# Kernel optimization log

Hardware: AMD Instinct MI355X
Metric: run time of the kernel (lower is better)

## Reference

```python
import jax, jax.numpy as jnp
import numpy as np

TT_SHAPES = [16, 16, 16, 16, 16, 16]
TT_RANKS = [1, 64, 64, 64, 64, 64, 1]
OUT_FEATURES = 4096  # 16*16*16
IN_FEATURES = 4096   # 16*16*16
N_TOKENS = 8192


def setup_inputs() -> dict:
    key = jax.random.key(0)
    ks = jax.random.split(key, len(TT_SHAPES) + 2)
    inp = {}
    for i in range(len(TT_SHAPES)):
        shape = (TT_RANKS[i], TT_SHAPES[i], TT_RANKS[i + 1])
        # xavier-uniform-like init
        fan = TT_RANKS[i] * TT_SHAPES[i] + TT_SHAPES[i] * TT_RANKS[i + 1]
        bound = float(np.sqrt(6.0 / fan))
        inp[f"core{i}"] = jax.random.uniform(ks[i], shape, jnp.float32, -bound, bound)
    inp["x"] = jax.random.normal(ks[-2], (N_TOKENS, IN_FEATURES), dtype=jnp.float32)
    b_bound = 1.0 / np.sqrt(IN_FEATURES)
    inp["b"] = jax.random.uniform(ks[-1], (OUT_FEATURES,), jnp.float32, -b_bound, b_bound)
    return inp


def _recover_weight(cores):
    # chain of reshape+matmul contractions, exactly as TTLinearR._recover_weight
    w = cores[0]
    for i in range(1, len(cores)):
        w = w.reshape(-1, TT_RANKS[i]) @ cores[i].reshape(TT_RANKS[i], -1)
    return w.reshape(OUT_FEATURES, IN_FEATURES)


def reference(x, core0, core1, core2, core3, core4, core5, b):
    w = _recover_weight([core0, core1, core2, core3, core4, core5])
    # F.linear(x, w, b) == x @ w.T + b
    return x @ w.T + b
```

## Files before the change

### kernel.cpp

```cpp
#include <hip/hip_runtime.h>


#define TOK 8192
#define DIN 4096
#define DOUT 4096
#define RNK 64

typedef __bf16 bf16x8 __attribute__((ext_vector_type(8)));
typedef float f32x4 __attribute__((ext_vector_type(4)));
typedef float f32x16 __attribute__((ext_vector_type(16)));

__device__ __forceinline__ unsigned short f2bf(float f) {
  unsigned int u = __float_as_uint(f);
  u += 0x7FFFu + ((u >> 16) & 1u);
  return (unsigned short)(u >> 16);
}

__global__ void chain1(const float* __restrict__ c0, const float* __restrict__ c1,
                       const float* __restrict__ c4, const float* __restrict__ c5,
                       float* __restrict__ S1, float* __restrict__ S3) {
  int b = blockIdx.x;
  if (b < 64) {
    int idx = b * 256 + threadIdx.x;
    int m = idx >> 10, n = idx & 1023;
    const float* a = c0 + m * 64;
    float acc = 0.f;
#pragma unroll
    for (int k = 0; k < 64; ++k) acc += a[k] * c1[k * 1024 + n];
    S1[idx] = acc;
  } else {
    int idx = (b - 64) * 256 + threadIdx.x;
    int m = idx >> 4, n = idx & 15;
    const float* a = c4 + m * 64;
    float acc = 0.f;
#pragma unroll
    for (int k = 0; k < 64; ++k) acc += a[k] * c5[k * 16 + n];
    S3[idx] = acc;
  }
}

__global__ void chain2(const float* __restrict__ S1, const float* __restrict__ c2,
                       const float* __restrict__ c3, const float* __restrict__ S3,
                       unsigned short* __restrict__ Abf, unsigned short* __restrict__ Bbf) {
  int b = blockIdx.x;
  if (b < 1024) {
    int idx = b * 256 + threadIdx.x;
    int m = idx >> 10, n = idx & 1023;
    const float* a = S1 + m * 64;
    float acc = 0.f;
#pragma unroll
    for (int k = 0; k < 64; ++k) acc += a[k] * c2[k * 1024 + n];
    Abf[idx] = f2bf(acc);
  } else {
    int idx = (b - 1024) * 256 + threadIdx.x;
    int m = idx >> 8, n = idx & 255;
    const float* a = c3 + m * 64;
    float acc = 0.f;
#pragma unroll
    for (int k = 0; k < 64; ++k) acc += a[k] * S3[k * 256 + n];
    Bbf[idx] = f2bf(acc);
  }
}

__global__ __launch_bounds__(512, 4)
void gemm1_s(const float* __restrict__ x, const unsigned short* __restrict__ Bbf,
             unsigned short* __restrict__ tb) {
  __shared__ float red[8 * 1024];

  const int tid = threadIdx.x;
  const int m0 = blockIdx.x * 16;
  const int lane = tid & 63, wv = tid >> 6;
  const int r = lane & 15, q = lane >> 4;
  const size_t xrow = (size_t)(m0 + r) * DIN;
  const int k0w = wv * 512;

  f32x4 acc[4];
#pragma unroll
  for (int j = 0; j < 4; ++j) acc[j] = (f32x4){0.f, 0.f, 0.f, 0.f};

#pragma unroll
  for (int st = 0; st < 16; ++st) {
    const int k0 = k0w + st * 32 + q * 8;
    float4 xa = *(const float4*)&x[xrow + k0];
    float4 xb = *(const float4*)&x[xrow + k0 + 4];
    bf16x8 a;
    a[0] = (__bf16)xa.x; a[1] = (__bf16)xa.y; a[2] = (__bf16)xa.z; a[3] = (__bf16)xa.w;
    a[4] = (__bf16)xb.x; a[5] = (__bf16)xb.y; a[6] = (__bf16)xb.z; a[7] = (__bf16)xb.w;
#pragma unroll
    for (int j = 0; j < 4; ++j) {
      bf16x8 b = *(const bf16x8*)&Bbf[(size_t)(j * 16 + r) * DIN + k0];
      acc[j] = __builtin_amdgcn_mfma_f32_16x16x32_bf16(a, b, acc[j], 0, 0, 0);
    }
  }

  float* myred = red + wv * 1024;
#pragma unroll
  for (int j = 0; j < 4; ++j)
#pragma unroll
    for (int g = 0; g < 4; ++g)
      myred[(q * 4 + g) * 64 + j * 16 + r] = acc[j][g];
  __syncthreads();

  const int o = tid * 2;
  float s0 = 0.f, s1 = 0.f;
#pragma unroll
  for (int w = 0; w < 8; ++w) {
    s0 += red[w * 1024 + o];
    s1 += red[w * 1024 + o + 1];
  }
  ushort2 h = {f2bf(s0), f2bf(s1)};
  *(ushort2*)&tb[(size_t)m0 * RNK + o] = h;
}

__global__ __launch_bounds__(256, 4)
void gemm2_s(const unsigned short* __restrict__ tb, const unsigned short* __restrict__ Abf,
             const float* __restrict__ bias, float* __restrict__ out) {
  const int tid = threadIdx.x;
  const int lane = tid & 63, wv = tid >> 6;
  const int l31 = lane & 31, hi = lane >> 5;
  const int n0 = blockIdx.x * 128;
  const int mb = blockIdx.y * 256;

  float bb[4];
#pragma unroll
  for (int n = 0; n < 4; ++n) bb[n] = bias[n0 + n * 32 + l31];

#pragma unroll 1
  for (int s = 0; s < 2; ++s) {
    const int m0 = mb + s * 128 + wv * 32;
    bf16x8 ta[4];
#pragma unroll
    for (int ks = 0; ks < 4; ++ks)
      ta[ks] = *(const bf16x8*)&tb[(size_t)(m0 + l31) * RNK + ks * 16 + hi * 8];

#pragma unroll 1
    for (int np = 0; np < 2; ++np) {
      f32x16 acc[2];
#pragma unroll
      for (int j = 0; j < 2; ++j)
#pragma unroll
        for (int e = 0; e < 16; ++e) acc[j][e] = 0.f;

#pragma unroll
      for (int ks = 0; ks < 4; ++ks) {
#pragma unroll
        for (int j = 0; j < 2; ++j) {
          const int nrow = n0 + (np * 2 + j) * 32 + l31;
          bf16x8 b = *(const bf16x8*)&Abf[(size_t)nrow * RNK + ks * 16 + hi * 8];
          acc[j] = __builtin_amdgcn_mfma_f32_32x32x16_bf16(ta[ks], b, acc[j], 0, 0, 0);
        }
      }

#pragma unroll
      for (int j = 0; j < 2; ++j) {
        const int col = n0 + (np * 2 + j) * 32 + l31;
        const float bj = bb[np * 2 + j];
#pragma unroll
        for (int reg = 0; reg < 16; ++reg) {
          const int rowt = (reg & 3) + 8 * (reg >> 2) + 4 * hi;
          out[(size_t)(m0 + rowt) * DOUT + col] = acc[j][reg] + bj;
        }
      }
    }
  }
}

extern "C" void kernel_launch(void* const* d_in, const int* in_sizes, int n_in,
                              void* d_out, int out_size, void* d_ws, size_t ws_size,
                              hipStream_t stream) {
  const float* c0 = (const float*)d_in[0];
  const float* c1 = (const float*)d_in[1];
  const float* c2 = (const float*)d_in[2];
  const float* c3 = (const float*)d_in[3];
  const float* c4 = (const float*)d_in[4];
  const float* c5 = (const float*)d_in[5];
  const float* x  = (const float*)d_in[6];
  const float* bias = (const float*)d_in[7];
  float* out = (float*)d_out;

  char* ws = (char*)d_ws;
  float*          S1  = (float*)(ws);
  float*          S3  = (float*)(ws + (1u << 16));
  unsigned short* Abf = (unsigned short*)(ws + (2u << 16));
  unsigned short* Bbf = (unsigned short*)(ws + (2u << 16) + (1u << 19));
  unsigned short* tbf = (unsigned short*)(ws + (2u << 16) + (2u << 19));

  chain1<<<128, 256, 0, stream>>>(c0, c1, c4, c5, S1, S3);
  chain2<<<2048, 256, 0, stream>>>(S1, c2, c3, S3, Abf, Bbf);
  gemm1_s<<<TOK / 16, 512, 0, stream>>>(x, Bbf, tbf);
  gemm2_s<<<dim3(DOUT / 128, TOK / 256), 256, 0, stream>>>(tbf, Abf, bias, out);
}
```

Measured before the change: 283.5 us.

## Software-pipeline gemm1 loads and stage gemm2 operands through padded LDS tiles

gemm1 now double-buffers its x and Bbf register loads, so the next K-step's global loads are issued while the current MFMAs run, hiding load latency. gemm2 is restructured into 128x256 output tiles handled by 512-thread blocks. Each block stages its token-rank and weight-factor slices into padded shared memory once, instead of having every wave reload them from global memory. This adds LDS use and a barrier, and the larger tiles may lower occupancy for the output-store-bound second GEMM.

```diff
diff --git a/kernel.cpp b/kernel.cpp
--- a/kernel.cpp
+++ b/kernel.cpp
@@ -5,6 +5,10 @@
 #define DIN 4096
 #define DOUT 4096
 #define RNK 64
+
+#define G2M 128
+#define G2N 256
+#define AS 72
 
 typedef __bf16 bf16x8 __attribute__((ext_vector_type(8)));
 typedef float f32x4 __attribute__((ext_vector_type(4)));
@@ -63,7 +67,7 @@
 }
 
 __global__ __launch_bounds__(512, 4)
-void gemm1_s(const float* __restrict__ x, const unsigned short* __restrict__ Bbf,
+void gemm1_p(const float* __restrict__ x, const unsigned short* __restrict__ Bbf,
              unsigned short* __restrict__ tb) {
   __shared__ float red[8 * 1024];
 
@@ -71,27 +75,60 @@
   const int m0 = blockIdx.x * 16;
   const int lane = tid & 63, wv = tid >> 6;
   const int r = lane & 15, q = lane >> 4;
-  const size_t xrow = (size_t)(m0 + r) * DIN;
-  const int k0w = wv * 512;
+  const float* xp = x + (size_t)(m0 + r) * DIN + wv * 512 + q * 8;
+  const unsigned short* bp = Bbf + (size_t)r * DIN + wv * 512 + q * 8;
 
   f32x4 acc[4];
 #pragma unroll
   for (int j = 0; j < 4; ++j) acc[j] = (f32x4){0.f, 0.f, 0.f, 0.f};
 
-#pragma unroll
-  for (int st = 0; st < 16; ++st) {
-    const int k0 = k0w + st * 32 + q * 8;
-    float4 xa = *(const float4*)&x[xrow + k0];
-    float4 xb = *(const float4*)&x[xrow + k0 + 4];
-    bf16x8 a;
-    a[0] = (__bf16)xa.x; a[1] = (__bf16)xa.y; a[2] = (__bf16)xa.z; a[3] = (__bf16)xa.w;
-    a[4] = (__bf16)xb.x; a[5] = (__bf16)xb.y; a[6] = (__bf16)xb.z; a[7] = (__bf16)xb.w;
-#pragma unroll
-    for (int j = 0; j < 4; ++j) {
-      bf16x8 b = *(const bf16x8*)&Bbf[(size_t)(j * 16 + r) * DIN + k0];
-      acc[j] = __builtin_amdgcn_mfma_f32_16x16x32_bf16(a, b, acc[j], 0, 0, 0);
-    }
-  }
+  float4 xa0 = *(const float4*)(xp);
+  float4 xb0 = *(const float4*)(xp + 4);
+  float4 xa1 = *(const float4*)(xp + 32);
+  float4 xb1 = *(const float4*)(xp + 36);
+  bf16x8 b0[4], b1[4];
+#pragma unroll
+  for (int j = 0; j < 4; ++j) {
+    b0[j] = *(const bf16x8*)(bp + (size_t)j * 16 * DIN);
+    b1[j] = *(const bf16x8*)(bp + (size_t)j * 16 * DIN + 32);
+  }
+
+#define G1_MFMA(XA, XB, BB)                                                      \
+  {                                                                              \
+    bf16x8 a;                                                                    \
+    a[0] = (__bf16)XA.x; a[1] = (__bf16)XA.y;                                    \
+    a[2] = (__bf16)XA.z; a[3] = (__bf16)XA.w;                                    \
+    a[4] = (__bf16)XB.x; a[5] = (__bf16)XB.y;                                    \
+    a[6] = (__bf16)XB.z; a[7] = (__bf16)XB.w;                                    \
+    _Pragma("unroll")                                                            \
+    for (int j = 0; j < 4; ++j)                                                  \
+      acc[j] = __builtin_amdgcn_mfma_f32_16x16x32_bf16(a, BB[j], acc[j], 0, 0, 0); \
+  }
+
+#pragma unroll 1
+  for (int st = 0; st < 14; st += 2) {
+    G1_MFMA(xa0, xb0, b0);
+    {
+      const float* xn = xp + (st + 2) * 32;
+      const unsigned short* bn = bp + (st + 2) * 32;
+      xa0 = *(const float4*)(xn);
+      xb0 = *(const float4*)(xn + 4);
+#pragma unroll
+      for (int j = 0; j < 4; ++j) b0[j] = *(const bf16x8*)(bn + (size_t)j * 16 * DIN);
+    }
+    G1_MFMA(xa1, xb1, b1);
+    {
+      const float* xn = xp + (st + 3) * 32;
+      const unsigned short* bn = bp + (st + 3) * 32;
+      xa1 = *(const float4*)(xn);
+      xb1 = *(const float4*)(xn + 4);
+#pragma unroll
+      for (int j = 0; j < 4; ++j) b1[j] = *(const bf16x8*)(bn + (size_t)j * 16 * DIN);
+    }
+  }
+  G1_MFMA(xa0, xb0, b0);
+  G1_MFMA(xa1, xb1, b1);
+#undef G1_MFMA
 
   float* myred = red + wv * 1024;
 #pragma unroll
@@ -112,55 +149,60 @@
   *(ushort2*)&tb[(size_t)m0 * RNK + o] = h;
 }
 
-__global__ __launch_bounds__(256, 4)
-void gemm2_s(const unsigned short* __restrict__ tb, const unsigned short* __restrict__ Abf,
+__global__ __launch_bounds__(512)
+void gemm2_y(const unsigned short* __restrict__ tbf, const unsigned short* __restrict__ Abf,
              const float* __restrict__ bias, float* __restrict__ out) {
+  __shared__ __align__(16) unsigned short sm[(G2M + G2N) * AS];
+  unsigned short* ts = sm;
+  unsigned short* as_ = sm + G2M * AS;
+
   const int tid = threadIdx.x;
+  const int m0 = blockIdx.y * G2M, n0 = blockIdx.x * G2N;
   const int lane = tid & 63, wv = tid >> 6;
   const int l31 = lane & 31, hi = lane >> 5;
-  const int n0 = blockIdx.x * 128;
-  const int mb = blockIdx.y * 256;
+  const int mw = (wv >> 1) * 32, nw = (wv & 1) * 128;
+
+#pragma unroll
+  for (int j = 0; j < 2; ++j) {
+    int f = j * 512 + tid;
+    int row = f >> 3, c = f & 7;
+    *(uint4*)&ts[row * AS + c * 8] = *(const uint4*)&tbf[(size_t)(m0 + row) * RNK + c * 8];
+  }
+#pragma unroll
+  for (int j = 0; j < 4; ++j) {
+    int f = j * 512 + tid;
+    int row = f >> 3, c = f & 7;
+    *(uint4*)&as_[row * AS + c * 8] = *(const uint4*)&Abf[(size_t)(n0 + row) * RNK + c * 8];
+  }
+  __syncthreads();
+
+  f32x16 acc[4];
+#pragma unroll
+  for (int j = 0; j < 4; ++j)
+#pragma unroll
+    for (int e = 0; e < 16; ++e) acc[j][e] = 0.f;
+
+#pragma unroll
+  for (int ks = 0; ks < 4; ++ks) {
+    bf16x8 a = *(const bf16x8*)&ts[(mw + l31) * AS + ks * 16 + hi * 8];
+#pragma unroll
+    for (int j = 0; j < 4; ++j) {
+      bf16x8 b = *(const bf16x8*)&as_[(nw + j * 32 + l31) * AS + ks * 16 + hi * 8];
+      acc[j] = __builtin_amdgcn_mfma_f32_32x32x16_bf16(a, b, acc[j], 0, 0, 0);
+    }
+  }
 
   float bb[4];
 #pragma unroll
-  for (int n = 0; n < 4; ++n) bb[n] = bias[n0 + n * 32 + l31];
-
-#pragma unroll 1
-  for (int s = 0; s < 2; ++s) {
-    const int m0 = mb + s * 128 + wv * 32;
-    bf16x8 ta[4];
-#pragma unroll
-    for (int ks = 0; ks < 4; ++ks)
-      ta[ks] = *(const bf16x8*)&tb[(size_t)(m0 + l31) * RNK + ks * 16 + hi * 8];
-
-#pragma unroll 1
-    for (int np = 0; np < 2; ++np) {
-      f32x16 acc[2];
-#pragma unroll
-      for (int j = 0; j < 2; ++j)
-#pragma unroll
-        for (int e = 0; e < 16; ++e) acc[j][e] = 0.f;
-
-#pragma unroll
-      for (int ks = 0; ks < 4; ++ks) {
-#pragma unroll
-        for (int j = 0; j < 2; ++j) {
-          const int nrow = n0 + (np * 2 + j) * 32 + l31;
-          bf16x8 b = *(const bf16x8*)&Abf[(size_t)nrow * RNK + ks * 16 + hi * 8];
-          acc[j] = __builtin_amdgcn_mfma_f32_32x32x16_bf16(ta[ks], b, acc[j], 0, 0, 0);
-        }
-      }
-
-#pragma unroll
-      for (int j = 0; j < 2; ++j) {
-        const int col = n0 + (np * 2 + j) * 32 + l31;
-        const float bj = bb[np * 2 + j];
-#pragma unroll
-        for (int reg = 0; reg < 16; ++reg) {
-          const int rowt = (reg & 3) + 8 * (reg >> 2) + 4 * hi;
-          out[(size_t)(m0 + rowt) * DOUT + col] = acc[j][reg] + bj;
-        }
-      }
+  for (int j = 0; j < 4; ++j) bb[j] = bias[n0 + nw + j * 32 + l31];
+
+#pragma unroll
+  for (int j = 0; j < 4; ++j) {
+    const int col = n0 + nw + j * 32 + l31;
+#pragma unroll
+    for (int reg = 0; reg < 16; ++reg) {
+      int rowt = (reg & 3) + 8 * (reg >> 2) + 4 * hi;
+      out[(size_t)(m0 + mw + rowt) * DOUT + col] = acc[j][reg] + bb[j];
     }
   }
 }
@@ -187,6 +229,6 @@
 
   chain1<<<128, 256, 0, stream>>>(c0, c1, c4, c5, S1, S3);
   chain2<<<2048, 256, 0, stream>>>(S1, c2, c3, S3, Abf, Bbf);
-  gemm1_s<<<TOK / 16, 512, 0, stream>>>(x, Bbf, tbf);
-  gemm2_s<<<dim3(DOUT / 128, TOK / 256), 256, 0, stream>>>(tbf, Abf, bias, out);
-}
+  gemm1_p<<<TOK / 16, 512, 0, stream>>>(x, Bbf, tbf);
+  gemm2_y<<<dim3(DOUT / G2N, TOK / G2M), 512, 0, stream>>>(tbf, Abf, bias, out);
+}
```

Result: no change. 280.6 us (-1.0%).
